# Kernel tuning notes

Hardware: AMD Instinct MI355X
Metric: run time of the kernel (lower is better)

Reference implementation:

```python
import jax, jax.numpy as jnp
import numpy as np

CUTOFFS = [0, 19997, 39997, 199997, 267735]  # cutoff_ends
SIZES = [19997, 20000, 160000, 67738]
DEMBS = [1024, 256, 64, 16]  # d_embed // div_val**i, div_val=4
N, D_PROJ = 1024, 1024


def setup_inputs() -> dict:
    key = jax.random.key(0)
    ks = jax.random.split(key, 20)
    inp = {
        "hidden": jax.random.normal(ks[0], (N, D_PROJ), jnp.float32),
        "target": jax.random.randint(ks[1], (N,), 0, CUTOFFS[-1], dtype=jnp.int64),
    }
    for i in range(4):
        inp[f"W{i}"] = 0.02 * jax.random.normal(ks[2 + 3 * i], (SIZES[i], DEMBS[i]), jnp.float32)
        inp[f"b{i}"] = jnp.zeros((SIZES[i],), jnp.float32)
        inp[f"p{i}"] = 0.02 * jax.random.normal(ks[3 + 3 * i], (D_PROJ, DEMBS[i]), jnp.float32)
    inp["cluster_weight"] = 0.02 * jax.random.normal(ks[14], (3, DEMBS[0]), jnp.float32)
    inp["cluster_bias"] = jnp.zeros((3,), jnp.float32)
    return inp


def _logit(hidden, W, b, p):
    # einsum('bd,de,ev->bv', hidden, proj, weight.T) + bias
    return (hidden @ p) @ W.T + b


def reference(hidden, target, W0, b0, p0, W1, b1, p1, W2, b2, p2, W3, b3, p3,
              cluster_weight, cluster_bias):
    n = hidden.shape[0]
    rows = jnp.arange(n)
    shortlist = W0.shape[0]  # 19997

    # head cluster: shortlist vocab + 3 cluster logits
    head_w = jnp.concatenate([W0, cluster_weight], axis=0)   # [shortlist+3, d_embed]
    head_b = jnp.concatenate([b0, cluster_bias], axis=0)
    head_lp = jax.nn.log_softmax(_logit(hidden, head_w, head_b, p0), axis=-1)  # [N, shortlist+3]

    masks = [target < CUTOFFS[1]]
    lps = [head_lp[rows, jnp.clip(target, 0, shortlist - 1)]]

    for i, (W, b, p) in enumerate([(W1, b1, p1), (W2, b2, p2), (W3, b3, p3)], start=1):
        l_idx, r_idx = CUTOFFS[i], CUTOFFS[i + 1]
        tail_lp = jax.nn.log_softmax(_logit(hidden, W, b, p), axis=-1)  # [N, r-l]
        rel = jnp.clip(target - l_idx, 0, r_idx - l_idx - 1)
        lps.append(head_lp[:, shortlist + i - 1] + tail_lp[rows, rel])
        masks.append((target >= l_idx) & (target < r_idx))

    logprob = jnp.select(masks, lps)
    return -logprob  # nll, shape [N]
```

## Files before the change

kernel.cpp:

```cpp
#include <hip/hip_runtime.h>
#include <stdint.h>

typedef short v8s __attribute__((ext_vector_type(8)));
typedef float f4 __attribute__((ext_vector_type(4)));
typedef unsigned short u16;
typedef unsigned int u32;

#define CUT1 19997
#define CUT2 39997
#define CUT3 199997
#define NROWS 1024
#define LDP 1360

__device__ __forceinline__ u32 pack2(float a, float b) {
    return (__float_as_uint(a) >> 16) | (__float_as_uint(b) & 0xffff0000u);
}
__device__ __forceinline__ float b2f(u16 h) { return __uint_as_float(((u32)h) << 16); }
__device__ __forceinline__ u16 f2b(float f) { return (u16)(__float_as_uint(f) >> 16); }

__device__ __forceinline__ void gload16(const void* g, void* l) {
    __builtin_amdgcn_global_load_lds(
        (const __attribute__((address_space(1))) u32*)g,
        (__attribute__((address_space(3))) u32*)l, 16, 0, 0);
}

__device__ __forceinline__ void cast8(const float* __restrict__ in, u16* __restrict__ out, size_t j) {
    const float4* p = (const float4*)(in + j * 8);
    float4 a = p[0], b = p[1];
    uint4 o = { pack2(a.x, a.y), pack2(a.z, a.w), pack2(b.x, b.y), pack2(b.z, b.w) };
    *(uint4*)(out + j * 8) = o;
}

#define H_E0 131072
#define H_E1 2690688
#define H_E2 3330688
#define H_E3 4610688
#define PREP_CAST_BLKS 18276
#define PREP_TR_BLKS 1376
__global__ __launch_bounds__(256) void prep_k(
    const float* __restrict__ hidden,
    const float* __restrict__ W0, const float* __restrict__ W1,
    const float* __restrict__ W2, const float* __restrict__ W3,
    const float* __restrict__ p0, const float* __restrict__ p1,
    const float* __restrict__ p2, const float* __restrict__ p3,
    const int* __restrict__ target,
    u16* __restrict__ hb, u16* __restrict__ W0b, u16* __restrict__ W1b,
    u16* __restrict__ W2b, u16* __restrict__ W3b, u16* __restrict__ pTb,
    float* __restrict__ rs, int* __restrict__ cnt, int* __restrict__ slot,
    int* __restrict__ rowmap)
{
    int bid = blockIdx.x;
    int tid = threadIdx.x;

    if (bid < PREP_CAST_BLKS) {
        int i = bid * 256 + tid;
        if (i < H_E0) { cast8(hidden, hb, i); return; }
        if (i < H_E1) { cast8(W0, W0b, i - H_E0); return; }
        if (i < H_E2) { cast8(W1, W1b, i - H_E1); return; }
        if (i < H_E3) { cast8(W2, W2b, i - H_E2); return; }
        int r = i - H_E3;
        if (r >= 67738) return;
        const float4* p = (const float4*)(W3 + (size_t)r * 16);
        float4 a = p[0], b = p[1], c = p[2], d = p[3];
        uint4 o0 = { pack2(a.x, a.y), pack2(a.z, a.w), pack2(b.x, b.y), pack2(b.z, b.w) };
        uint4 o1 = { pack2(c.x, c.y), pack2(c.z, c.w), pack2(d.x, d.y), pack2(d.z, d.w) };
        uint4 z = { 0, 0, 0, 0 };
        uint4* q = (uint4*)(W3b + (size_t)r * 32);
        q[0] = o0; q[1] = o1; q[2] = z; q[3] = z;
        return;
    }

    if (bid < PREP_CAST_BLKS + PREP_TR_BLKS) {
        int b = bid - PREP_CAST_BLKS;
        const float* src; int d, rowOff, bx, by;
        if (b < 1024)      { src = p0; d = 1024; rowOff = 0;    bx = b & 31;          by = b >> 5; }
        else if (b < 1280) { src = p1; d = 256;  rowOff = 1024; bx = (b - 1024) & 7;  by = (b - 1024) >> 3; }
        else if (b < 1344) { src = p2; d = 64;   rowOff = 1280; bx = (b - 1280) & 1;  by = (b - 1280) >> 1; }
        else               { src = p3; d = 16;   rowOff = 1344; bx = 0;               by = b - 1344; }
        __shared__ float tile[32][33];
        int tx = tid & 31, ty = tid >> 5;
        int x = bx * 32 + tx;
        int ybase = by * 32;
#pragma unroll
        for (int j = 0; j < 4; ++j) {
            int r = ty + j * 8;
            tile[r][tx] = (x < d) ? src[(size_t)(ybase + r) * d + x] : 0.f;
        }
        __syncthreads();
#pragma unroll
        for (int j = 0; j < 4; ++j) {
            int x2 = bx * 32 + ty + j * 8;
            if (x2 < d) pTb[(size_t)(rowOff + x2) * 1024 + ybase + tx] = f2b(tile[tx][ty + j * 8]);
        }
        return;
    }

    __shared__ int lcnt[3];
    for (int i = tid; i < 4096; i += 256) rs[i] = 0.f;
    for (int i = tid; i < 3072; i += 256) rowmap[i] = 0;
    if (tid < 3) lcnt[tid] = 0;
    __syncthreads();
    for (int r = tid; r < NROWS; r += 256) {
        int t = target[r];
        int c = (t < CUT1) ? -1 : (t < CUT2) ? 0 : (t < CUT3) ? 1 : 2;
        int s = -1;
        if (c >= 0) {
            s = atomicAdd(&lcnt[c], 1);
            rowmap[c * 1024 + s] = r;
        }
        slot[r] = s;
    }
    __syncthreads();
    if (tid < 3) cnt[tid] = lcnt[tid];
}

template<int MODE>
__device__ __forceinline__ void gemm_body(
    const u16* __restrict__ A, int lda, const int* __restrict__ rowmap,
    const u16* __restrict__ B, int ldb,
    const float* __restrict__ bias, int N, int K,
    u16* __restrict__ Cout, int ldc,
    float* __restrict__ rowsum, const int* __restrict__ count,
    int bx, int by)
{
    __shared__ __align__(16) u16 As[4096];
    __shared__ __align__(16) u16 Bs[4096];

    const int tid = threadIdx.x;
    const int rbase = bx * 128, cbase = by * 128;
    if (MODE == 1 && count) {
        int c = *count;
        if (rbase >= ((c + 127) & ~127)) return;
    }

    const int wave = tid >> 6, lane = tid & 63;
    const int l4 = lane & 15, quad = lane >> 4;
    const int wg = (wave >> 1) * 4;
    const int cg = (wave & 1) * 4;

    const u16 *Asrc0, *Asrc1, *Bsrc0, *Bsrc1;
    {
        int s0 = tid, s1 = 256 + tid;
        int g0 = s0 >> 6, seg0 = (s0 >> 4) & 3, r0 = s0 & 15;
        int g1 = s1 >> 6, seg1 = (s1 >> 4) & 3, r1 = s1 & 15;
        int ar0 = rbase + g0 * 16 + r0, ar1 = rbase + g1 * 16 + r1;
        if (rowmap) { ar0 = rowmap[ar0]; ar1 = rowmap[ar1]; }
        Asrc0 = A + (size_t)ar0 * lda + seg0 * 8;
        Asrc1 = A + (size_t)ar1 * lda + seg1 * 8;
        int bc0 = cbase + g0 * 16 + r0; if (bc0 >= N) bc0 = N - 1;
        int bc1 = cbase + g1 * 16 + r1; if (bc1 >= N) bc1 = N - 1;
        Bsrc0 = B + (size_t)bc0 * ldb + seg0 * 8;
        Bsrc1 = B + (size_t)bc1 * ldb + seg1 * 8;
    }
    u16* Ad0 = &As[tid * 8]; u16* Ad1 = &As[(256 + tid) * 8];
    u16* Bd0 = &Bs[tid * 8]; u16* Bd1 = &Bs[(256 + tid) * 8];

    f4 acc[4][4] = {};
    for (int kk = 0; kk < K; kk += 32) {
        gload16(Asrc0 + kk, Ad0);
        gload16(Asrc1 + kk, Ad1);
        gload16(Bsrc0 + kk, Bd0);
        gload16(Bsrc1 + kk, Bd1);
        __syncthreads();
        v8s af[4], bf[4];
#pragma unroll
        for (int r = 0; r < 4; ++r)
            af[r] = *(const v8s*)&As[((wg + r) * 64 + quad * 16 + l4) * 8];
#pragma unroll
        for (int c = 0; c < 4; ++c)
            bf[c] = *(const v8s*)&Bs[((cg + c) * 64 + quad * 16 + l4) * 8];
#pragma unroll
        for (int r = 0; r < 4; ++r)
#pragma unroll
            for (int c = 0; c < 4; ++c)
                acc[r][c] = __builtin_amdgcn_mfma_f32_16x16x32_bf16(af[r], bf[c], acc[r][c], 0, 0, 0);
        __syncthreads();
    }

    const int wr = wg * 16, wc = cg * 16;
    if (MODE == 0) {
#pragma unroll
        for (int c = 0; c < 4; ++c) {
            int col = cbase + wc + c * 16 + l4;
            if (col < N) {
#pragma unroll
                for (int r = 0; r < 4; ++r)
#pragma unroll
                    for (int g = 0; g < 4; ++g) {
                        int row = rbase + wr + r * 16 + quad * 4 + g;
                        Cout[(size_t)row * ldc + col] = f2b(acc[r][c][g]);
                    }
            }
        }
    } else {
        float part[4][4];
#pragma unroll
        for (int r = 0; r < 4; ++r)
#pragma unroll
            for (int g = 0; g < 4; ++g) part[r][g] = 0.f;
#pragma unroll
        for (int c = 0; c < 4; ++c) {
            int col = cbase + wc + c * 16 + l4;
            if (col < N) {
                float bb = bias[col];
#pragma unroll
                for (int r = 0; r < 4; ++r)
#pragma unroll
                    for (int g = 0; g < 4; ++g)
                        part[r][g] += __expf(acc[r][c][g] + bb);
            }
        }
#pragma unroll
        for (int off = 1; off < 16; off <<= 1)
#pragma unroll
            for (int r = 0; r < 4; ++r)
#pragma unroll
                for (int g = 0; g < 4; ++g)
                    part[r][g] += __shfl_xor(part[r][g], off);
        float v = part[0][0];
#pragma unroll
        for (int r = 0; r < 4; ++r)
#pragma unroll
            for (int g = 0; g < 4; ++g)
                if (l4 == r * 4 + g) v = part[r][g];
        int row = rbase + wr + (l4 >> 2) * 16 + quad * 4 + (l4 & 3);
        atomicAdd(&rowsum[row], v);
    }
}

__global__ __launch_bounds__(256) void proj_gemm_k(
    const u16* __restrict__ hb, const u16* __restrict__ pTb, u16* __restrict__ proj)
{
    int bid = blockIdx.x;
    gemm_body<0>(hb, 1024, nullptr, pTb, 1024, nullptr, 1360, 1024,
                 proj, LDP, nullptr, nullptr, bid & 7, bid >> 3);
}

#define SE_GRID 16752
__global__ __launch_bounds__(256) void sumexp_k(
    const u16* __restrict__ proj,
    const u16* __restrict__ W0b, const u16* __restrict__ W1b,
    const u16* __restrict__ W2b, const u16* __restrict__ W3b,
    const float* __restrict__ b0, const float* __restrict__ b1,
    const float* __restrict__ b2, const float* __restrict__ b3,
    float* __restrict__ rs, const int* __restrict__ rmap, const int* __restrict__ cnt)
{
    int bid = blockIdx.x;
    const u16 *A, *B; const float* bias; float* rsum;
    const int *rm, *cn; int N, K, ldb, rel;
    if (bid < 1256) {
        A = proj;        rm = nullptr;     cn = nullptr;  B = W0b; ldb = 1024;
        bias = b0; N = CUT1;   K = 1024; rsum = rs;        rel = bid;
    } else if (bid < 2512) {
        A = proj + 1024; rm = rmap;        cn = cnt;      B = W1b; ldb = 256;
        bias = b1; N = 20000;  K = 256;  rsum = rs + 1024; rel = bid - 1256;
    } else if (bid < 12512) {
        A = proj + 1280; rm = rmap + 1024; cn = cnt + 1;  B = W2b; ldb = 64;
        bias = b2; N = 160000; K = 64;   rsum = rs + 2048; rel = bid - 2512;
    } else {
        A = proj + 1344; rm = rmap + 2048; cn = cnt + 2;  B = W3b; ldb = 32;
        bias = b3; N = 67738;  K = 32;   rsum = rs + 3072; rel = bid - 12512;
    }
    gemm_body<1>(A, LDP, rm, B, ldb, bias, N, K, nullptr, 0, rsum, cn, rel & 7, rel >> 3);
}

__global__ __launch_bounds__(256) void final_k(
    const u16* __restrict__ proj, const int* __restrict__ target, const int* __restrict__ slot,
    const float* __restrict__ cw, const float* __restrict__ cb,
    const float* __restrict__ W0, const float* __restrict__ b0,
    const float* __restrict__ W1, const float* __restrict__ b1,
    const float* __restrict__ W2, const float* __restrict__ b2,
    const float* __restrict__ W3, const float* __restrict__ b3,
    const float* __restrict__ rs, float* __restrict__ out)
{
    int row = blockIdx.x * 4 + (threadIdx.x >> 6);
    int lane = threadIdx.x & 63;
    const u16* pr = proj + (size_t)row * LDP;

    float c0 = 0.f, c1 = 0.f, c2 = 0.f;
    for (int k = lane; k < 1024; k += 64) {
        float pv = b2f(pr[k]);
        c0 += pv * cw[k]; c1 += pv * cw[1024 + k]; c2 += pv * cw[2048 + k];
    }
#pragma unroll
    for (int off = 1; off < 64; off <<= 1) {
        c0 += __shfl_xor(c0, off); c1 += __shfl_xor(c1, off); c2 += __shfl_xor(c2, off);
    }

    int t = target[row];
    const float* W; const float* bb; int K, off, rel;
    if (t < CUT1)      { W = W0; bb = b0; K = 1024; off = 0;    rel = t; }
    else if (t < CUT2) { W = W1; bb = b1; K = 256;  off = 1024; rel = t - CUT1; }
    else if (t < CUT3) { W = W2; bb = b2; K = 64;   off = 1280; rel = t - CUT2; }
    else               { W = W3; bb = b3; K = 16;   off = 1344; rel = t - CUT3; }
    float acc = 0.f;
    const float* wr = W + (size_t)rel * K;
    for (int k = lane; k < K; k += 64) acc += b2f(pr[off + k]) * wr[k];
#pragma unroll
    for (int o2 = 1; o2 < 64; o2 <<= 1) acc += __shfl_xor(acc, o2);

    if (lane == 0) {
        c0 += cb[0]; c1 += cb[1]; c2 += cb[2];
        float tl = acc + bb[rel];
        float lseh = __logf(rs[row] + __expf(c0) + __expf(c1) + __expf(c2));
        float lp;
        if (t < CUT1) lp = tl - lseh;
        else {
            int c = (t < CUT2) ? 0 : (t < CUT3) ? 1 : 2;
            float cc = (c == 0) ? c0 : (c == 1) ? c1 : c2;
            lp = (cc - lseh) + (tl - __logf(rs[(c + 1) * 1024 + slot[row]]));
        }
        out[row] = -lp;
    }
}

__global__ void cast_bf16_k(const float* __restrict__ in, u16* __restrict__ out, int n8) {
    int i = blockIdx.x * 256 + threadIdx.x;
    if (i >= n8) return;
    cast8(in, out, i);
}

__global__ void transpose_f_k(const float* __restrict__ in, float* __restrict__ out, int d, int rowOff) {
    __shared__ float tile[32][33];
    int tx = threadIdx.x, ty = threadIdx.y;
    int x = blockIdx.x * 32 + tx;
    int ybase = blockIdx.y * 32;
#pragma unroll
    for (int j = 0; j < 4; ++j) {
        int r = ty + j * 8;
        tile[r][tx] = (x < d) ? in[(size_t)(ybase + r) * d + x] : 0.f;
    }
    __syncthreads();
#pragma unroll
    for (int j = 0; j < 4; ++j) {
        int x2 = blockIdx.x * 32 + ty + j * 8;
        if (x2 < d) out[(size_t)(rowOff + x2) * 1024 + ybase + tx] = tile[tx][ty + j * 8];
    }
}

__global__ __launch_bounds__(256) void gemm_tn_k(
    const u16* __restrict__ A, int lda,
    const float* __restrict__ B, int ldb,
    const float* __restrict__ bias, int N, int K,
    u16* __restrict__ Cout, int ldc, float* __restrict__ rowsum)
{
    int tid = threadIdx.x;
    int wave = tid >> 6, lane = tid & 63;
    int l4 = lane & 15, quad = lane >> 4;
    int rbase = blockIdx.x * 16;
    int cbase = blockIdx.y * 256 + wave * 64;

    f4 acc[4] = {};
    v8s zero8 = {0, 0, 0, 0, 0, 0, 0, 0};
    const u16* arow = A + (size_t)(rbase + l4) * lda;
    int nk = (K + 31) >> 5;
    for (int kt = 0; kt < nk; ++kt) {
        int kk = (kt << 5) + quad * 8;
        v8s a = (kk < K) ? *(const v8s*)(arow + kk) : zero8;
#pragma unroll
        for (int t = 0; t < 4; ++t) {
            int col = cbase + t * 16 + l4;
            v8s b = zero8;
            if ((col < N) && (kk < K)) {
                const float* bp = B + (size_t)col * ldb + kk;
                float4 f0 = *(const float4*)bp;
                float4 f1 = *(const float4*)(bp + 4);
                union { uint4 u; v8s s; } bu;
                bu.u.x = pack2(f0.x, f0.y); bu.u.y = pack2(f0.z, f0.w);
                bu.u.z = pack2(f1.x, f1.y); bu.u.w = pack2(f1.z, f1.w);
                b = bu.s;
            }
            acc[t] = __builtin_amdgcn_mfma_f32_16x16x32_bf16(a, b, acc[t], 0, 0, 0);
        }
    }
    if (Cout) {
#pragma unroll
        for (int t = 0; t < 4; ++t) {
            int col = cbase + t * 16 + l4;
            if (col < N) {
#pragma unroll
                for (int r = 0; r < 4; ++r)
                    Cout[(size_t)(rbase + quad * 4 + r) * ldc + col] = f2b(acc[t][r]);
            }
        }
    } else {
        float part[4] = {0.f, 0.f, 0.f, 0.f};
#pragma unroll
        for (int t = 0; t < 4; ++t) {
            int col = cbase + t * 16 + l4;
            if (col < N) {
                float bb = bias[col];
#pragma unroll
                for (int r = 0; r < 4; ++r) part[r] += __expf(acc[t][r] + bb);
            }
        }
#pragma unroll
        for (int off = 1; off < 16; off <<= 1)
#pragma unroll
            for (int r = 0; r < 4; ++r) part[r] += __shfl_xor(part[r], off);
        if (l4 < 4) {
            float v = (l4 == 0) ? part[0] : (l4 == 1) ? part[1] : (l4 == 2) ? part[2] : part[3];
            atomicAdd(&rowsum[rbase + quad * 4 + l4], v);
        }
    }
}

__global__ __launch_bounds__(256) void gather_k(
    const u16* __restrict__ proj, const int* __restrict__ target,
    const float* __restrict__ cw, const float* __restrict__ cb,
    const float* __restrict__ W0, const float* __restrict__ b0,
    const float* __restrict__ W1, const float* __restrict__ b1,
    const float* __restrict__ W2, const float* __restrict__ b2,
    const float* __restrict__ W3, const float* __restrict__ b3,
    float* __restrict__ rs_head, float* __restrict__ cl, float* __restrict__ tl)
{
    int row = blockIdx.x * 4 + (threadIdx.x >> 6);
    int lane = threadIdx.x & 63;
    const u16* pr = proj + (size_t)row * LDP;

    float c0 = 0.f, c1 = 0.f, c2 = 0.f;
    for (int k = lane; k < 1024; k += 64) {
        float pv = b2f(pr[k]);
        c0 += pv * cw[k]; c1 += pv * cw[1024 + k]; c2 += pv * cw[2048 + k];
    }
#pragma unroll
    for (int off = 1; off < 64; off <<= 1) {
        c0 += __shfl_xor(c0, off); c1 += __shfl_xor(c1, off); c2 += __shfl_xor(c2, off);
    }
    int t = target[row];
    const float* W; const float* bb; int K, off, rel;
    if (t < CUT1)      { W = W0; bb = b0; K = 1024; off = 0;    rel = t; }
    else if (t < CUT2) { W = W1; bb = b1; K = 256;  off = 1024; rel = t - CUT1; }
    else if (t < CUT3) { W = W2; bb = b2; K = 64;   off = 1280; rel = t - CUT2; }
    else               { W = W3; bb = b3; K = 16;   off = 1344; rel = t - CUT3; }
    float acc = 0.f;
    const float* wr = W + (size_t)rel * K;
    for (int k = lane; k < K; k += 64) acc += b2f(pr[off + k]) * wr[k];
#pragma unroll
    for (int o2 = 1; o2 < 64; o2 <<= 1) acc += __shfl_xor(acc, o2);
    if (lane == 0) {
        c0 += cb[0]; c1 += cb[1]; c2 += cb[2];
        cl[row * 3 + 0] = c0; cl[row * 3 + 1] = c1; cl[row * 3 + 2] = c2;
        atomicAdd(&rs_head[row], __expf(c0) + __expf(c1) + __expf(c2));
        tl[row] = acc + bb[rel];
    }
}

__global__ void finalize_full_k(const int* __restrict__ target, const float* __restrict__ rs,
                                const float* __restrict__ cl, const float* __restrict__ tl,
                                float* __restrict__ out)
{
    int i = blockIdx.x * 256 + threadIdx.x;
    if (i >= NROWS) return;
    int t = target[i];
    float lseh = __logf(rs[i]);
    float lp;
    if (t < CUT1) lp = tl[i] - lseh;
    else {
        int c = (t < CUT2) ? 0 : (t < CUT3) ? 1 : 2;
        lp = (cl[i * 3 + c] - lseh) + (tl[i] - __logf(rs[(c + 1) * 1024 + i]));
    }
    out[i] = -lp;
}

extern "C" void kernel_launch(void* const* d_in, const int* in_sizes, int n_in,
                              void* d_out, int out_size, void* d_ws, size_t ws_size,
                              hipStream_t stream)
{
    const float* hidden = (const float*)d_in[0];
    const int*   target = (const int*)d_in[1];
    const float* W0 = (const float*)d_in[2];
    const float* b0 = (const float*)d_in[3];
    const float* p0 = (const float*)d_in[4];
    const float* W1 = (const float*)d_in[5];
    const float* b1 = (const float*)d_in[6];
    const float* p1 = (const float*)d_in[7];
    const float* W2 = (const float*)d_in[8];
    const float* b2 = (const float*)d_in[9];
    const float* p2 = (const float*)d_in[10];
    const float* W3 = (const float*)d_in[11];
    const float* b3 = (const float*)d_in[12];
    const float* p3 = (const float*)d_in[13];
    const float* cw = (const float*)d_in[14];
    const float* cb = (const float*)d_in[15];
    float* out = (float*)d_out;
    char* w = (char*)d_ws;

    if (ws_size >= 84000000ull) {
        u16*   hb   = (u16*)(w + 0);
        u16*   pTb  = (u16*)(w + 2097152);
        u16*   proj = (u16*)(w + 4882432);
        u16*   W0b  = (u16*)(w + 7667712);
        u16*   W1b  = (u16*)(w + 48621568);
        u16*   W2b  = (u16*)(w + 58861568);
        u16*   W3b  = (u16*)(w + 79341568);
        float* rs   = (float*)(w + 83676800);
        int*   cnt  = (int*)(w + 83693184);
        int*   slot = (int*)(w + 83693200);
        int*   rmap = (int*)(w + 83697296);

        prep_k<<<PREP_CAST_BLKS + PREP_TR_BLKS + 1, 256, 0, stream>>>(
            hidden, W0, W1, W2, W3, p0, p1, p2, p3, target,
            hb, W0b, W1b, W2b, W3b, pTb, rs, cnt, slot, rmap);

        proj_gemm_k<<<88, 256, 0, stream>>>(hb, pTb, proj);

        sumexp_k<<<SE_GRID, 256, 0, stream>>>(proj, W0b, W1b, W2b, W3b,
                                              b0, b1, b2, b3, rs, rmap, cnt);

        final_k<<<256, 256, 0, stream>>>(proj, target, slot, cw, cb,
                                         W0, b0, W1, b1, W2, b2, W3, b3, rs, out);
    } else {
        float* pT   = (float*)w;
        u16*   hb   = (u16*)(w + 5570560);
        u16*   proj = (u16*)(w + 7667712);
        float* rs   = (float*)(w + 10452992);
        float* cl   = (float*)(w + 10469376);
        float* tl   = (float*)(w + 10481664);
        dim3 tb(32, 8);

        hipMemsetAsync(rs, 0, 4 * 1024 * sizeof(float), stream);
        cast_bf16_k<<<512, 256, 0, stream>>>(hidden, hb, 131072);
        transpose_f_k<<<dim3(32, 32), tb, 0, stream>>>(p0, pT, 1024, 0);
        transpose_f_k<<<dim3(8, 32),  tb, 0, stream>>>(p1, pT, 256, 1024);
        transpose_f_k<<<dim3(2, 32),  tb, 0, stream>>>(p2, pT, 64, 1280);
        transpose_f_k<<<dim3(1, 32),  tb, 0, stream>>>(p3, pT, 16, 1344);

        gemm_tn_k<<<dim3(64, 6), 256, 0, stream>>>(hb, 1024, pT, 1024, nullptr,
                                                   1360, 1024, proj, LDP, nullptr);
        gemm_tn_k<<<dim3(64, 79), 256, 0, stream>>>(proj, LDP, W0, 1024, b0,
                                                    CUT1, 1024, nullptr, 0, rs);
        gemm_tn_k<<<dim3(64, 79), 256, 0, stream>>>(proj + 1024, LDP, W1, 256, b1,
                                                    20000, 256, nullptr, 0, rs + 1024);
        gemm_tn_k<<<dim3(64, 625), 256, 0, stream>>>(proj + 1280, LDP, W2, 64, b2,
                                                     160000, 64, nullptr, 0, rs + 2048);
        gemm_tn_k<<<dim3(64, 265), 256, 0, stream>>>(proj + 1344, LDP, W3, 16, b3,
                                                     67738, 16, nullptr, 0, rs + 3072);

        gather_k<<<256, 256, 0, stream>>>(proj, target, cw, cb,
                                          W0, b0, W1, b1, W2, b2, W3, b3, rs, cl, tl);
        finalize_full_k<<<4, 256, 0, stream>>>(target, rs, cl, tl, out);
    }
}
```

Measured before the change: 443.2 us.

## Overlap weight casts with projection GEMM and batch tail column tiles per block

The big weight fp32→bf16 casts move out of the prep kernel and into the same launch as the projection GEMM. The 88 GEMM blocks can then run alongside the cast blocks instead of after them. The tail-cluster sumexp blocks now loop over 4 or 8 column tiles each, keeping per-row partial sums in registers. This cuts the grid from 16752 to 3368 blocks, reducing early-exit block overhead and atomic row-sum traffic. The cost is less parallelism per tail cluster and longer-running blocks.

```diff
diff --git a/kernel.cpp b/kernel.cpp
--- a/kernel.cpp
+++ b/kernel.cpp
@@ -31,47 +31,24 @@
     *(uint4*)(out + j * 8) = o;
 }
 
-#define H_E0 131072
-#define H_E1 2690688
-#define H_E2 3330688
-#define H_E3 4610688
-#define PREP_CAST_BLKS 18276
-#define PREP_TR_BLKS 1376
-__global__ __launch_bounds__(256) void prep_k(
+__global__ __launch_bounds__(256) void prep_small_k(
     const float* __restrict__ hidden,
-    const float* __restrict__ W0, const float* __restrict__ W1,
-    const float* __restrict__ W2, const float* __restrict__ W3,
     const float* __restrict__ p0, const float* __restrict__ p1,
     const float* __restrict__ p2, const float* __restrict__ p3,
     const int* __restrict__ target,
-    u16* __restrict__ hb, u16* __restrict__ W0b, u16* __restrict__ W1b,
-    u16* __restrict__ W2b, u16* __restrict__ W3b, u16* __restrict__ pTb,
+    u16* __restrict__ hb, u16* __restrict__ pTb,
     float* __restrict__ rs, int* __restrict__ cnt, int* __restrict__ slot,
     int* __restrict__ rowmap)
 {
     int bid = blockIdx.x;
     int tid = threadIdx.x;
 
-    if (bid < PREP_CAST_BLKS) {
-        int i = bid * 256 + tid;
-        if (i < H_E0) { cast8(hidden, hb, i); return; }
-        if (i < H_E1) { cast8(W0, W0b, i - H_E0); return; }
-        if (i < H_E2) { cast8(W1, W1b, i - H_E1); return; }
-        if (i < H_E3) { cast8(W2, W2b, i - H_E2); return; }
-        int r = i - H_E3;
-        if (r >= 67738) return;
-        const float4* p = (const float4*)(W3 + (size_t)r * 16);
-        float4 a = p[0], b = p[1], c = p[2], d = p[3];
-        uint4 o0 = { pack2(a.x, a.y), pack2(a.z, a.w), pack2(b.x, b.y), pack2(b.z, b.w) };
-        uint4 o1 = { pack2(c.x, c.y), pack2(c.z, c.w), pack2(d.x, d.y), pack2(d.z, d.w) };
-        uint4 z = { 0, 0, 0, 0 };
-        uint4* q = (uint4*)(W3b + (size_t)r * 32);
-        q[0] = o0; q[1] = o1; q[2] = z; q[3] = z;
+    if (bid < 512) {
+        cast8(hidden, hb, bid * 256 + tid);
         return;
     }
-
-    if (bid < PREP_CAST_BLKS + PREP_TR_BLKS) {
-        int b = bid - PREP_CAST_BLKS;
+    if (bid < 1888) {
+        int b = bid - 512;
         const float* src; int d, rowOff, bx, by;
         if (b < 1024)      { src = p0; d = 1024; rowOff = 0;    bx = b & 31;          by = b >> 5; }
         else if (b < 1280) { src = p1; d = 256;  rowOff = 1024; bx = (b - 1024) & 7;  by = (b - 1024) >> 3; }
@@ -114,20 +91,18 @@
     if (tid < 3) cnt[tid] = lcnt[tid];
 }
 
-template<int MODE>
+template<int MODE, int NCOL>
 __device__ __forceinline__ void gemm_body(
+    u16* __restrict__ As, u16* __restrict__ Bs,
     const u16* __restrict__ A, int lda, const int* __restrict__ rowmap,
     const u16* __restrict__ B, int ldb,
     const float* __restrict__ bias, int N, int K,
     u16* __restrict__ Cout, int ldc,
     float* __restrict__ rowsum, const int* __restrict__ count,
-    int bx, int by)
-{
-    __shared__ __align__(16) u16 As[4096];
-    __shared__ __align__(16) u16 Bs[4096];
-
+    int bx, int byg)
+{
     const int tid = threadIdx.x;
-    const int rbase = bx * 128, cbase = by * 128;
+    const int rbase = bx * 128;
     if (MODE == 1 && count) {
         int c = *count;
         if (rbase >= ((c + 127) & ~127)) return;
@@ -138,78 +113,90 @@
     const int wg = (wave >> 1) * 4;
     const int cg = (wave & 1) * 4;
 
-    const u16 *Asrc0, *Asrc1, *Bsrc0, *Bsrc1;
+    const int g0 = tid >> 6, seg0 = (tid >> 4) & 3, r0 = tid & 15;
+    const int s1 = 256 + tid;
+    const int g1 = s1 >> 6, seg1 = (s1 >> 4) & 3, r1 = s1 & 15;
+
+    const u16 *Asrc0, *Asrc1;
     {
-        int s0 = tid, s1 = 256 + tid;
-        int g0 = s0 >> 6, seg0 = (s0 >> 4) & 3, r0 = s0 & 15;
-        int g1 = s1 >> 6, seg1 = (s1 >> 4) & 3, r1 = s1 & 15;
         int ar0 = rbase + g0 * 16 + r0, ar1 = rbase + g1 * 16 + r1;
         if (rowmap) { ar0 = rowmap[ar0]; ar1 = rowmap[ar1]; }
         Asrc0 = A + (size_t)ar0 * lda + seg0 * 8;
         Asrc1 = A + (size_t)ar1 * lda + seg1 * 8;
+    }
+    u16* Ad0 = &As[tid * 8]; u16* Ad1 = &As[(256 + tid) * 8];
+    u16* Bd0 = &Bs[tid * 8]; u16* Bd1 = &Bs[(256 + tid) * 8];
+
+    float part[4][4];
+    if (MODE == 1) {
+#pragma unroll
+        for (int r = 0; r < 4; ++r)
+#pragma unroll
+            for (int g = 0; g < 4; ++g) part[r][g] = 0.f;
+    }
+
+    const int wr = wg * 16, wc = cg * 16;
+
+    for (int ct = 0; ct < NCOL; ++ct) {
+        const int cbase = (byg * NCOL + ct) * 128;
         int bc0 = cbase + g0 * 16 + r0; if (bc0 >= N) bc0 = N - 1;
         int bc1 = cbase + g1 * 16 + r1; if (bc1 >= N) bc1 = N - 1;
-        Bsrc0 = B + (size_t)bc0 * ldb + seg0 * 8;
-        Bsrc1 = B + (size_t)bc1 * ldb + seg1 * 8;
-    }
-    u16* Ad0 = &As[tid * 8]; u16* Ad1 = &As[(256 + tid) * 8];
-    u16* Bd0 = &Bs[tid * 8]; u16* Bd1 = &Bs[(256 + tid) * 8];
-
-    f4 acc[4][4] = {};
-    for (int kk = 0; kk < K; kk += 32) {
-        gload16(Asrc0 + kk, Ad0);
-        gload16(Asrc1 + kk, Ad1);
-        gload16(Bsrc0 + kk, Bd0);
-        gload16(Bsrc1 + kk, Bd1);
-        __syncthreads();
-        v8s af[4], bf[4];
-#pragma unroll
-        for (int r = 0; r < 4; ++r)
-            af[r] = *(const v8s*)&As[((wg + r) * 64 + quad * 16 + l4) * 8];
-#pragma unroll
-        for (int c = 0; c < 4; ++c)
-            bf[c] = *(const v8s*)&Bs[((cg + c) * 64 + quad * 16 + l4) * 8];
-#pragma unroll
-        for (int r = 0; r < 4; ++r)
+        const u16* Bsrc0 = B + (size_t)bc0 * ldb + seg0 * 8;
+        const u16* Bsrc1 = B + (size_t)bc1 * ldb + seg1 * 8;
+
+        f4 acc[4][4] = {};
+        for (int kk = 0; kk < K; kk += 32) {
+            gload16(Asrc0 + kk, Ad0);
+            gload16(Asrc1 + kk, Ad1);
+            gload16(Bsrc0 + kk, Bd0);
+            gload16(Bsrc1 + kk, Bd1);
+            __syncthreads();
+            v8s af[4], bf[4];
+#pragma unroll
+            for (int r = 0; r < 4; ++r)
+                af[r] = *(const v8s*)&As[((wg + r) * 64 + quad * 16 + l4) * 8];
 #pragma unroll
             for (int c = 0; c < 4; ++c)
-                acc[r][c] = __builtin_amdgcn_mfma_f32_16x16x32_bf16(af[r], bf[c], acc[r][c], 0, 0, 0);
-        __syncthreads();
-    }
-
-    const int wr = wg * 16, wc = cg * 16;
-    if (MODE == 0) {
-#pragma unroll
-        for (int c = 0; c < 4; ++c) {
-            int col = cbase + wc + c * 16 + l4;
-            if (col < N) {
-#pragma unroll
-                for (int r = 0; r < 4; ++r)
-#pragma unroll
-                    for (int g = 0; g < 4; ++g) {
-                        int row = rbase + wr + r * 16 + quad * 4 + g;
-                        Cout[(size_t)row * ldc + col] = f2b(acc[r][c][g]);
-                    }
+                bf[c] = *(const v8s*)&Bs[((cg + c) * 64 + quad * 16 + l4) * 8];
+#pragma unroll
+            for (int r = 0; r < 4; ++r)
+#pragma unroll
+                for (int c = 0; c < 4; ++c)
+                    acc[r][c] = __builtin_amdgcn_mfma_f32_16x16x32_bf16(af[r], bf[c], acc[r][c], 0, 0, 0);
+            __syncthreads();
+        }
+
+        if (MODE == 0) {
+#pragma unroll
+            for (int c = 0; c < 4; ++c) {
+                int col = cbase + wc + c * 16 + l4;
+                if (col < N) {
+#pragma unroll
+                    for (int r = 0; r < 4; ++r)
+#pragma unroll
+                        for (int g = 0; g < 4; ++g) {
+                            int row = rbase + wr + r * 16 + quad * 4 + g;
+                            Cout[(size_t)row * ldc + col] = f2b(acc[r][c][g]);
+                        }
+                }
             }
-        }
-    } else {
-        float part[4][4];
-#pragma unroll
-        for (int r = 0; r < 4; ++r)
-#pragma unroll
-            for (int g = 0; g < 4; ++g) part[r][g] = 0.f;
-#pragma unroll
-        for (int c = 0; c < 4; ++c) {
-            int col = cbase + wc + c * 16 + l4;
-            if (col < N) {
-                float bb = bias[col];
-#pragma unroll
-                for (int r = 0; r < 4; ++r)
-#pragma unroll
-                    for (int g = 0; g < 4; ++g)
-                        part[r][g] += __expf(acc[r][c][g] + bb);
+        } else {
+#pragma unroll
+            for (int c = 0; c < 4; ++c) {
+                int col = cbase + wc + c * 16 + l4;
+                if (col < N) {
+                    float bb = bias[col];
+#pragma unroll
+                    for (int r = 0; r < 4; ++r)
+#pragma unroll
+                        for (int g = 0; g < 4; ++g)
+                            part[r][g] += __expf(acc[r][c][g] + bb);
+                }
             }
         }
+    }
+
+    if (MODE == 1) {
 #pragma unroll
         for (int off = 1; off < 16; off <<= 1)
 #pragma unroll
@@ -228,15 +215,40 @@
     }
 }
 
-__global__ __launch_bounds__(256) void proj_gemm_k(
-    const u16* __restrict__ hb, const u16* __restrict__ pTb, u16* __restrict__ proj)
-{
+#define CP_E0 2559616
+#define CP_E1 3199616
+#define CP_E2 4479616
+__global__ __launch_bounds__(256) void castproj_k(
+    const u16* __restrict__ hb, const u16* __restrict__ pTb, u16* __restrict__ proj,
+    const float* __restrict__ W0, const float* __restrict__ W1,
+    const float* __restrict__ W2, const float* __restrict__ W3,
+    u16* __restrict__ W0b, u16* __restrict__ W1b,
+    u16* __restrict__ W2b, u16* __restrict__ W3b)
+{
+    __shared__ __align__(16) u16 As[4096];
+    __shared__ __align__(16) u16 Bs[4096];
     int bid = blockIdx.x;
-    gemm_body<0>(hb, 1024, nullptr, pTb, 1024, nullptr, 1360, 1024,
-                 proj, LDP, nullptr, nullptr, bid & 7, bid >> 3);
-}
-
-#define SE_GRID 16752
+    if (bid < 88) {
+        gemm_body<0, 1>(As, Bs, hb, 1024, nullptr, pTb, 1024, nullptr, 1360, 1024,
+                        proj, LDP, nullptr, nullptr, bid & 7, bid >> 3);
+        return;
+    }
+    int i = (bid - 88) * 256 + threadIdx.x;
+    if (i < CP_E0) { cast8(W0, W0b, i); return; }
+    if (i < CP_E1) { cast8(W1, W1b, i - CP_E0); return; }
+    if (i < CP_E2) { cast8(W2, W2b, i - CP_E1); return; }
+    int r = i - CP_E2;
+    if (r >= 67738) return;
+    const float4* p = (const float4*)(W3 + (size_t)r * 16);
+    float4 a = p[0], b = p[1], c = p[2], d = p[3];
+    uint4 o0 = { pack2(a.x, a.y), pack2(a.z, a.w), pack2(b.x, b.y), pack2(b.z, b.w) };
+    uint4 o1 = { pack2(c.x, c.y), pack2(c.z, c.w), pack2(d.x, d.y), pack2(d.z, d.w) };
+    uint4 z = { 0, 0, 0, 0 };
+    uint4* q = (uint4*)(W3b + (size_t)r * 32);
+    q[0] = o0; q[1] = o1; q[2] = z; q[3] = z;
+}
+
+#define SE_GRID 3368
 __global__ __launch_bounds__(256) void sumexp_k(
     const u16* __restrict__ proj,
     const u16* __restrict__ W0b, const u16* __restrict__ W1b,
@@ -245,23 +257,25 @@
     const float* __restrict__ b2, const float* __restrict__ b3,
     float* __restrict__ rs, const int* __restrict__ rmap, const int* __restrict__ cnt)
 {
+    __shared__ __align__(16) u16 As[4096];
+    __shared__ __align__(16) u16 Bs[4096];
     int bid = blockIdx.x;
-    const u16 *A, *B; const float* bias; float* rsum;
-    const int *rm, *cn; int N, K, ldb, rel;
     if (bid < 1256) {
-        A = proj;        rm = nullptr;     cn = nullptr;  B = W0b; ldb = 1024;
-        bias = b0; N = CUT1;   K = 1024; rsum = rs;        rel = bid;
-    } else if (bid < 2512) {
-        A = proj + 1024; rm = rmap;        cn = cnt;      B = W1b; ldb = 256;
-        bias = b1; N = 20000;  K = 256;  rsum = rs + 1024; rel = bid - 1256;
-    } else if (bid < 12512) {
-        A = proj + 1280; rm = rmap + 1024; cn = cnt + 1;  B = W2b; ldb = 64;
-        bias = b2; N = 160000; K = 64;   rsum = rs + 2048; rel = bid - 2512;
+        gemm_body<1, 1>(As, Bs, proj, LDP, nullptr, W0b, 1024, b0, CUT1, 1024,
+                        nullptr, 0, rs, nullptr, bid & 7, bid >> 3);
+    } else if (bid < 1576) {
+        int rel = bid - 1256;
+        gemm_body<1, 4>(As, Bs, proj + 1024, LDP, rmap, W1b, 256, b1, 20000, 256,
+                        nullptr, 0, rs + 1024, cnt + 0, rel & 7, rel >> 3);
+    } else if (bid < 2832) {
+        int rel = bid - 1576;
+        gemm_body<1, 8>(As, Bs, proj + 1280, LDP, rmap + 1024, W2b, 64, b2, 160000, 64,
+                        nullptr, 0, rs + 2048, cnt + 1, rel & 7, rel >> 3);
     } else {
-        A = proj + 1344; rm = rmap + 2048; cn = cnt + 2;  B = W3b; ldb = 32;
-        bias = b3; N = 67738;  K = 32;   rsum = rs + 3072; rel = bid - 12512;
-    }
-    gemm_body<1>(A, LDP, rm, B, ldb, bias, N, K, nullptr, 0, rsum, cn, rel & 7, rel >> 3);
+        int rel = bid - 2832;
+        gemm_body<1, 8>(As, Bs, proj + 1344, LDP, rmap + 2048, W3b, 32, b3, 67738, 32,
+                        nullptr, 0, rs + 3072, cnt + 2, rel & 7, rel >> 3);
+    }
 }
 
 __global__ __launch_bounds__(256) void final_k(
@@ -499,11 +513,11 @@
         int*   slot = (int*)(w + 83693200);
         int*   rmap = (int*)(w + 83697296);
 
-        prep_k<<<PREP_CAST_BLKS + PREP_TR_BLKS + 1, 256, 0, stream>>>(
-            hidden, W0, W1, W2, W3, p0, p1, p2, p3, target,
-            hb, W0b, W1b, W2b, W3b, pTb, rs, cnt, slot, rmap);
-
-        proj_gemm_k<<<88, 256, 0, stream>>>(hb, pTb, proj);
+        prep_small_k<<<1889, 256, 0, stream>>>(hidden, p0, p1, p2, p3, target,
+                                               hb, pTb, rs, cnt, slot, rmap);
+
+        castproj_k<<<17852, 256, 0, stream>>>(hb, pTb, proj,
+                                              W0, W1, W2, W3, W0b, W1b, W2b, W3b);
 
         sumexp_k<<<SE_GRID, 256, 0, stream>>>(proj, W0b, W1b, W2b, W3b,
                                               b0, b1, b2, b3, rs, rmap, cnt);
```

Result: faster. 433.9 us (-2.1%).
